# Kernel tuning notes

Measured on AMD Instinct MI355X. Metric: run time of the kernel, lower is better.

## Reference

```python
import jax, jax.numpy as jnp
import numpy as np

N = 50000      # nodes
E = 800000     # edges (before self-loops)
H = 4          # attention heads
C = 64         # hidden_dim per head
F_IN = 8       # node_features
NEG_SLOPE = 0.2  # PyG GATConv default


def setup_inputs() -> dict:
    key = jax.random.key(0)
    ks = jax.random.split(key, 16)
    def g(k, shape, fan_in):
        return (jax.random.normal(k, shape, jnp.float32) / np.sqrt(fan_in)).astype(jnp.float32)
    x = jax.random.normal(ks[0], (N, F_IN), jnp.float32)
    edge_index = jax.random.randint(ks[1], (2, E), 0, N, dtype=jnp.int32)
    # GATConv params: layer 0 maps F_IN->H*C, layers 1,2 map H*C->H*C
    W0 = g(ks[2], (F_IN, H * C), F_IN)
    Ws = g(ks[3], (2, H * C, H * C), H * C)
    att_src = g(ks[4], (3, H, C), C)
    att_dst = g(ks[5], (3, H, C), C)
    bconv = jnp.zeros((3, H * C), jnp.float32)
    # order / time predictor MLPs: Linear(256,64) -> ReLU -> Linear(64,1)
    ow1 = g(ks[6], (H * C, C), H * C); ob1 = jnp.zeros((C,), jnp.float32)
    ow2 = g(ks[7], (C, 1), C);         ob2 = jnp.zeros((1,), jnp.float32)
    tw1 = g(ks[8], (H * C, C), H * C); tb1 = jnp.zeros((C,), jnp.float32)
    tw2 = g(ks[9], (C, 1), C);         tb2 = jnp.zeros((1,), jnp.float32)
    return {"x": x, "edge_index": edge_index, "W0": W0, "Ws": Ws,
            "att_src": att_src, "att_dst": att_dst, "bconv": bconv,
            "ow1": ow1, "ob1": ob1, "ow2": ow2, "ob2": ob2,
            "tw1": tw1, "tb1": tb1, "tw2": tw2, "tb2": tb2}


def _gat_layer(h_in, src, dst, W, a_src, a_dst, b):
    """PyG-style GATConv (concat heads, eval mode, self-loops already in src/dst)."""
    h = (h_in @ W).reshape(N, H, C)                       # [N,H,C]
    al_s = jnp.einsum('nhc,hc->nh', h, a_src)             # [N,H]
    al_d = jnp.einsum('nhc,hc->nh', h, a_dst)             # [N,H]
    e = jax.nn.leaky_relu(al_s[src] + al_d[dst], NEG_SLOPE)  # [Etot,H]
    m = jax.ops.segment_max(e, dst, num_segments=N)       # segment-softmax over in-edges
    ee = jnp.exp(e - m[dst])
    den = jax.ops.segment_sum(ee, dst, num_segments=N)
    alpha = ee / den[dst]                                 # [Etot,H]
    out = jax.ops.segment_sum(h[src] * alpha[:, :, None], dst, num_segments=N)
    return out.reshape(N, H * C) + b


def reference(x, edge_index, W0, Ws, att_src, att_dst, bconv,
              ow1, ob1, ow2, ob2, tw1, tb1, tw2, tb2):
    loops = jnp.arange(N, dtype=edge_index.dtype)
    src = jnp.concatenate([edge_index[0], loops])
    dst = jnp.concatenate([edge_index[1], loops])
    h = _gat_layer(x, src, dst, W0, att_src[0], att_dst[0], bconv[0])
    h = jax.nn.relu(h)   # dropout is identity in eval
    h = _gat_layer(h, src, dst, Ws[0], att_src[1], att_dst[1], bconv[1])
    h = jax.nn.relu(h)
    h = _gat_layer(h, src, dst, Ws[1], att_src[2], att_dst[2], bconv[2])
    order_scores = jax.nn.relu(h @ ow1 + ob1) @ ow2 + ob2  # [N,1]
    time_scores = jax.nn.relu(h @ tw1 + tb1) @ tw2 + tb2   # [N,1]
    return (order_scores, time_scores)
```

## Files before the change

kernel.cpp:

```cpp
#include <hip/hip_runtime.h>
#include <hip/hip_bf16.h>
#include <hip/hip_fp16.h>

#define NN 50000
#define EE 800000
#define ET 850000
#define HH 4
#define CC 64
#define HC 256
#define DMAX 128

using f16v8 = __attribute__((ext_vector_type(8))) _Float16;
using f32v4 = __attribute__((ext_vector_type(4))) float;

__device__ __forceinline__ float4 cvt_h4(uint2 raw) {
    __half2 a = *reinterpret_cast<__half2*>(&raw.x);
    __half2 b = *reinterpret_cast<__half2*>(&raw.y);
    float2 fa = __half22float2(a), fb = __half22float2(b);
    return make_float4(fa.x, fa.y, fb.x, fb.y);
}

__global__ void k_bucket(const int* __restrict__ ei, int* __restrict__ cnt,
                         int* __restrict__ esrc) {
    int e = blockIdx.x * blockDim.x + threadIdx.x;
    if (e < ET) {
        int d, s;
        if (e < EE) { d = ei[EE + e]; s = ei[e]; }
        else        { d = e - EE;     s = e - EE; }
        int pos = atomicAdd(&cnt[d], 1);
        if (pos < DMAX) esrc[d * DMAX + pos] = s;
    }
}

__global__ void k_prep(const float* __restrict__ Ws,
                       const float* __restrict__ ow1, const float* __restrict__ tw1,
                       __half* __restrict__ Wt, __half* __restrict__ Wh) {
    int i = blockIdx.x * 256 + threadIdx.x;
    if (i < 2 * HC * HC) {
        int m = i >> 16;
        int n = (i >> 8) & 255;
        int k = i & 255;
        Wt[i] = __float2half(Ws[m * HC * HC + k * HC + n]);
    }
    int j = i - 2 * HC * HC;
    if (j >= 0 && j < 128 * HC) {
        int c = j >> 8;
        int k = j & 255;
        float v = (c < 64) ? ow1[k * CC + c] : tw1[k * CC + (c - 64)];
        Wh[j] = __float2half(v);
    }
}

#define G0_NODES 16
__global__ __launch_bounds__(256) void k_gemm0(const float* __restrict__ x,
                                               const float* __restrict__ W0,
                                               const float* __restrict__ asrc,
                                               const float* __restrict__ adst,
                                               __half* __restrict__ hg,
                                               float* __restrict__ al_s,
                                               float* __restrict__ al_d) {
    __shared__ float sx[G0_NODES * 8];
    int t = threadIdx.x;
    int n0 = blockIdx.x * G0_NODES;
    float w[8];
#pragma unroll
    for (int k = 0; k < 8; k++) w[k] = W0[k * HC + t];
    float as = asrc[t], ad = adst[t];
    int lane = t & 63, wv = t >> 6;
    if (t < G0_NODES * 8) sx[t] = x[(size_t)n0 * 8 + t];
    __syncthreads();
    for (int ni = 0; ni < G0_NODES; ni++) {
        int n = n0 + ni;
        float acc = 0.f;
#pragma unroll
        for (int k = 0; k < 8; k++) acc += sx[ni * 8 + k] * w[k];
        hg[(size_t)n * HC + t] = __float2half(acc);
        float s = acc * as, d = acc * ad;
        for (int off = 32; off > 0; off >>= 1) {
            s += __shfl_down(s, off, 64);
            d += __shfl_down(d, off, 64);
        }
        if (lane == 0) { al_s[n * HH + wv] = s; al_d[n * HH + wv] = d; }
    }
}

#define GM 128
#define GN 128
#define GK 64
__global__ __launch_bounds__(256) void k_gemmh(const __half* __restrict__ A,
                                               const __half* __restrict__ Bt,
                                               const float* __restrict__ asrc,
                                               const float* __restrict__ adst,
                                               __half* __restrict__ hg,
                                               float* __restrict__ al_s,
                                               float* __restrict__ al_d) {
    __shared__ __half As[GM][GK + 8];
    __shared__ __half Bs[GN][GK + 8];
    int t = threadIdx.x;
    int l = t & 63, wv = t >> 6;
    int wm = wv >> 1, wn = wv & 1;
    int row0 = blockIdx.x * GM;
    int col0 = blockIdx.y * GN;
    f32v4 acc[4][4] = {};
    const __half* Ab = A + (size_t)row0 * HC;
    const __half* Bb = Bt + (size_t)col0 * HC;
    int sr = t >> 3, sc = (t & 7) * 8;
    for (int k0 = 0; k0 < HC; k0 += GK) {
#pragma unroll
        for (int i = 0; i < 4; i++) {
            int rr = sr + i * 32;
            uint4 v = {0u, 0u, 0u, 0u};
            if (row0 + rr < NN) v = *(const uint4*)(Ab + (size_t)rr * HC + k0 + sc);
            *(uint4*)&As[rr][sc] = v;
            *(uint4*)&Bs[rr][sc] = *(const uint4*)(Bb + (size_t)rr * HC + k0 + sc);
        }
        __syncthreads();
#pragma unroll
        for (int kk = 0; kk < GK; kk += 32) {
            f16v8 af[4], bf[4];
#pragma unroll
            for (int i = 0; i < 4; i++)
                af[i] = *(const f16v8*)&As[wm * 64 + i * 16 + (l & 15)][kk + (l >> 4) * 8];
#pragma unroll
            for (int j = 0; j < 4; j++)
                bf[j] = *(const f16v8*)&Bs[wn * 64 + j * 16 + (l & 15)][kk + (l >> 4) * 8];
#pragma unroll
            for (int i = 0; i < 4; i++)
#pragma unroll
                for (int j = 0; j < 4; j++)
                    acc[i][j] = __builtin_amdgcn_mfma_f32_16x16x32_f16(af[i], bf[j], acc[i][j], 0, 0, 0);
        }
        __syncthreads();
    }
    int head = (col0 >> 6) + wn;
    float va[4], vd[4];
#pragma unroll
    for (int j = 0; j < 4; j++) {
        int c = j * 16 + (l & 15);
        va[j] = asrc[head * CC + c];
        vd[j] = adst[head * CC + c];
    }
    int cbase = col0 + wn * 64 + (l & 15);
#pragma unroll
    for (int i = 0; i < 4; i++) {
#pragma unroll
        for (int v = 0; v < 4; v++) {
            int r = row0 + wm * 64 + i * 16 + (l >> 4) * 4 + v;
            bool ok = (r < NN);
            float s = 0.f, d = 0.f;
#pragma unroll
            for (int j = 0; j < 4; j++) {
                float xv = acc[i][j][v];
                s += xv * va[j];
                d += xv * vd[j];
                if (ok) hg[(size_t)r * HC + cbase + j * 16] = __float2half(xv);
            }
            s += __shfl_xor(s, 8, 16); d += __shfl_xor(d, 8, 16);
            s += __shfl_xor(s, 4, 16); d += __shfl_xor(d, 4, 16);
            s += __shfl_xor(s, 2, 16); d += __shfl_xor(d, 2, 16);
            s += __shfl_xor(s, 1, 16); d += __shfl_xor(d, 1, 16);
            if (ok && (l & 15) == 0) {
                al_s[r * HH + head] = s;
                al_d[r * HH + head] = d;
            }
        }
    }
}

__global__ __launch_bounds__(256) void k_fagg(const int* __restrict__ cnt,
                                              const int* __restrict__ esrc,
                                              const float* __restrict__ al_s,
                                              const float* __restrict__ al_d,
                                              const __half* __restrict__ hg,
                                              const float* __restrict__ bias,
                                              __half* __restrict__ out, int do_relu) {
    __shared__ float s_p[4][HH][72];
    __shared__ int   s_src[4][64];
    int t = threadIdx.x;
    int wv = t >> 6, l = t & 63;
    int n = blockIdx.x * 4 + wv;
    int myh = l >> 4;
    int beg = n * DMAX;
    int end = beg + cnt[n];
    float4 ad = *(const float4*)&al_d[(size_t)n * HH];
    float den = 0.f;
    float4 acc = {0.f, 0.f, 0.f, 0.f};
    const __half* hgl = hg + l * 4;

    for (int off = beg; off < end; off += 64) {
        int csize = min(64, end - off);
        float4 pp = {0.f, 0.f, 0.f, 0.f};
        int s = 0;
        if (l < csize) {
            s = esrc[off + l];
            float4 as = *(const float4*)&al_s[(size_t)s * HH];
            float v;
            v = as.x + ad.x; pp.x = __expf((v > 0.f) ? v : 0.2f * v);
            v = as.y + ad.y; pp.y = __expf((v > 0.f) ? v : 0.2f * v);
            v = as.z + ad.z; pp.z = __expf((v > 0.f) ? v : 0.2f * v);
            v = as.w + ad.w; pp.w = __expf((v > 0.f) ? v : 0.2f * v);
        }
        s_src[wv][l] = s;
        s_p[wv][0][l] = pp.x;
        s_p[wv][1][l] = pp.y;
        s_p[wv][2][l] = pp.z;
        s_p[wv][3][l] = pp.w;
        const float* prow = s_p[wv][myh];
        const int*   srow = s_src[wv];
        int k = 0;
        for (; k + 8 <= csize; k += 8) {
            int si[8];
#pragma unroll
            for (int u = 0; u < 8; u++) si[u] = srow[k + u];
            uint2 rw[8];
#pragma unroll
            for (int u = 0; u < 8; u++) rw[u] = *(const uint2*)&hgl[(size_t)si[u] * HC];
            float p[8];
#pragma unroll
            for (int u = 0; u < 8; u++) p[u] = prow[k + u];
#pragma unroll
            for (int u = 0; u < 8; u++) {
                float4 v = cvt_h4(rw[u]);
                den += p[u];
                acc.x += p[u] * v.x;
                acc.y += p[u] * v.y;
                acc.z += p[u] * v.z;
                acc.w += p[u] * v.w;
            }
        }
        for (; k + 4 <= csize; k += 4) {
            int si[4];
#pragma unroll
            for (int u = 0; u < 4; u++) si[u] = srow[k + u];
            uint2 rw[4];
#pragma unroll
            for (int u = 0; u < 4; u++) rw[u] = *(const uint2*)&hgl[(size_t)si[u] * HC];
            float p[4];
#pragma unroll
            for (int u = 0; u < 4; u++) p[u] = prow[k + u];
#pragma unroll
            for (int u = 0; u < 4; u++) {
                float4 v = cvt_h4(rw[u]);
                den += p[u];
                acc.x += p[u] * v.x;
                acc.y += p[u] * v.y;
                acc.z += p[u] * v.z;
                acc.w += p[u] * v.w;
            }
        }
        for (; k < csize; k++) {
            float p = prow[k];
            float4 v = cvt_h4(*(const uint2*)&hgl[(size_t)srow[k] * HC]);
            den += p;
            acc.x += p * v.x; acc.y += p * v.y; acc.z += p * v.z; acc.w += p * v.w;
        }
    }

    float4 b = *(const float4*)&bias[l * 4];
    float inv = 1.f / den;
    float4 o;
    o.x = acc.x * inv + b.x; o.y = acc.y * inv + b.y;
    o.z = acc.z * inv + b.z; o.w = acc.w * inv + b.w;
    if (do_relu) {
        o.x = fmaxf(o.x, 0.f); o.y = fmaxf(o.y, 0.f);
        o.z = fmaxf(o.z, 0.f); o.w = fmaxf(o.w, 0.f);
    }
    union { __half h[4]; uint2 u; } pk;
    pk.h[0] = __float2half(o.x); pk.h[1] = __float2half(o.y);
    pk.h[2] = __float2half(o.z); pk.h[3] = __float2half(o.w);
    *(uint2*)&out[(size_t)n * HC + l * 4] = pk.u;
}

__global__ __launch_bounds__(256) void k_headh(const __half* __restrict__ A,
                                               const __half* __restrict__ Wh,
                                               const float* __restrict__ ob1,
                                               const float* __restrict__ ow2,
                                               const float* __restrict__ ob2,
                                               const float* __restrict__ tb1,
                                               const float* __restrict__ tw2,
                                               const float* __restrict__ tb2,
                                               float* __restrict__ out) {
    __shared__ __half As[GM][GK + 8];
    __shared__ __half Bs[GN][GK + 8];
    int t = threadIdx.x;
    int l = t & 63, wv = t >> 6;
    int wm = wv >> 1, wn = wv & 1;
    int row0 = blockIdx.x * GM;
    f32v4 acc[4][4] = {};
    const __half* Ab = A + (size_t)row0 * HC;
    int sr = t >> 3, sc = (t & 7) * 8;
    for (int k0 = 0; k0 < HC; k0 += GK) {
#pragma unroll
        for (int i = 0; i < 4; i++) {
            int rr = sr + i * 32;
            uint4 v = {0u, 0u, 0u, 0u};
            if (row0 + rr < NN) v = *(const uint4*)(Ab + (size_t)rr * HC + k0 + sc);
            *(uint4*)&As[rr][sc] = v;
            *(uint4*)&Bs[rr][sc] = *(const uint4*)(Wh + (size_t)rr * HC + k0 + sc);
        }
        __syncthreads();
#pragma unroll
        for (int kk = 0; kk < GK; kk += 32) {
            f16v8 af[4], bf[4];
#pragma unroll
            for (int i = 0; i < 4; i++)
                af[i] = *(const f16v8*)&As[wm * 64 + i * 16 + (l & 15)][kk + (l >> 4) * 8];
#pragma unroll
            for (int j = 0; j < 4; j++)
                bf[j] = *(const f16v8*)&Bs[wn * 64 + j * 16 + (l & 15)][kk + (l >> 4) * 8];
#pragma unroll
            for (int i = 0; i < 4; i++)
#pragma unroll
                for (int j = 0; j < 4; j++)
                    acc[i][j] = __builtin_amdgcn_mfma_f32_16x16x32_f16(af[i], bf[j], acc[i][j], 0, 0, 0);
        }
        __syncthreads();
    }
    float b1[4], w2[4];
#pragma unroll
    for (int j = 0; j < 4; j++) {
        int c = j * 16 + (l & 15);
        b1[j] = wn ? tb1[c] : ob1[c];
        w2[j] = wn ? tw2[c] : ow2[c];
    }
    float b2 = wn ? tb2[0] : ob2[0];
#pragma unroll
    for (int i = 0; i < 4; i++) {
#pragma unroll
        for (int v = 0; v < 4; v++) {
            int r = row0 + wm * 64 + i * 16 + (l >> 4) * 4 + v;
            float s = 0.f;
#pragma unroll
            for (int j = 0; j < 4; j++)
                s += fmaxf(acc[i][j][v] + b1[j], 0.f) * w2[j];
            s += __shfl_xor(s, 8, 16);
            s += __shfl_xor(s, 4, 16);
            s += __shfl_xor(s, 2, 16);
            s += __shfl_xor(s, 1, 16);
            if ((l & 15) == 0 && r < NN)
                out[(size_t)(wn ? NN : 0) + r] = s + b2;
        }
    }
}

extern "C" void kernel_launch(void* const* d_in, const int* in_sizes, int n_in,
                              void* d_out, int out_size, void* d_ws, size_t ws_size,
                              hipStream_t stream) {
    const float* x      = (const float*)d_in[0];
    const int*   ei     = (const int*)d_in[1];
    const float* W0     = (const float*)d_in[2];
    const float* Ws     = (const float*)d_in[3];
    const float* attsrc = (const float*)d_in[4];
    const float* attdst = (const float*)d_in[5];
    const float* bconv  = (const float*)d_in[6];
    const float* ow1 = (const float*)d_in[7];
    const float* ob1 = (const float*)d_in[8];
    const float* ow2 = (const float*)d_in[9];
    const float* ob2 = (const float*)d_in[10];
    const float* tw1 = (const float*)d_in[11];
    const float* tb1 = (const float*)d_in[12];
    const float* tw2 = (const float*)d_in[13];
    const float* tb2 = (const float*)d_in[14];
    float* outp = (float*)d_out;

    char* ws = (char*)d_ws;
    size_t off = 0;
    auto alloc = [&](size_t bytes) -> void* {
        void* p = ws + off;
        off += (bytes + 255) & ~(size_t)255;
        return p;
    };
    __half*   hA      = (__half*)alloc(sizeof(__half) * NN * HC);
    __half*   hB16    = (__half*)alloc(sizeof(__half) * NN * HC);
    float*    al_s    = (float*)alloc(sizeof(float) * NN * HH);
    float*    al_d    = (float*)alloc(sizeof(float) * NN * HH);
    int*      cnt     = (int*)alloc(sizeof(int) * NN);
    int*      esrc    = (int*)alloc(sizeof(int) * (size_t)NN * DMAX);
    __half*   Wt      = (__half*)alloc(sizeof(__half) * 2 * HC * HC);
    __half*   Wh      = (__half*)alloc(sizeof(__half) * 128 * HC);
    (void)ws_size; (void)in_sizes; (void)n_in; (void)out_size;

    hipMemsetAsync(cnt, 0, sizeof(int) * NN, stream);
    k_bucket<<<(ET + 255) / 256, 256, 0, stream>>>(ei, cnt, esrc);
    k_prep<<<(2 * HC * HC + 128 * HC + 255) / 256, 256, 0, stream>>>(Ws, ow1, tw1, Wt, Wh);

    for (int l = 0; l < 3; l++) {
        if (l == 0) {
            k_gemm0<<<NN / G0_NODES, 256, 0, stream>>>(x, W0, attsrc, attdst,
                                                       hA, al_s, al_d);
        } else {
            dim3 grid((NN + GM - 1) / GM, 2);
            k_gemmh<<<grid, 256, 0, stream>>>(hB16, Wt + (size_t)(l - 1) * HC * HC,
                                              attsrc + l * HC, attdst + l * HC,
                                              hA, al_s, al_d);
        }
        k_fagg<<<NN / 4, 256, 0, stream>>>(cnt, esrc, al_s, al_d, hA,
                                           bconv + l * HC, hB16, (l < 2) ? 1 : 0);
    }

    k_headh<<<(NN + GM - 1) / GM, 256, 0, stream>>>(hB16, Wh, ob1, ow2, ob2,
                                                    tb1, tw2, tb2, outp);
}
```

Before: 364.9 us.

## Build compact CSR with 16-bit sources and split aggregation by column slice

Replaces the fixed 128-slot padded bucket with a CSR built from a count histogram, an atomic-cursor offset assignment and a scatter pass. Source indices are stored as 16-bit values, and the histogram and offset steps are fused into the weight-prep and layer-0 GEMM kernels. The aggregation kernel now gives each block one 32-column slice for 16 nodes, with 8 edges handled in parallel per wavefront and combined by a shuffle reduction. This is meant to shrink edge-list memory, drop the degree cap, and spread gather work more evenly. In exchange it adds an extra edge pass and reduction overhead, and the order of sources within a node's edge list is no longer deterministic.

```diff
diff --git a/kernel.cpp b/kernel.cpp
--- a/kernel.cpp
+++ b/kernel.cpp
@@ -8,7 +8,6 @@
 #define HH 4
 #define CC 64
 #define HC 256
-#define DMAX 128
 
 using f16v8 = __attribute__((ext_vector_type(8))) _Float16;
 using f32v4 = __attribute__((ext_vector_type(4))) float;
@@ -20,22 +19,20 @@
     return make_float4(fa.x, fa.y, fb.x, fb.y);
 }
 
-__global__ void k_bucket(const int* __restrict__ ei, int* __restrict__ cnt,
-                         int* __restrict__ esrc) {
-    int e = blockIdx.x * blockDim.x + threadIdx.x;
-    if (e < ET) {
-        int d, s;
-        if (e < EE) { d = ei[EE + e]; s = ei[e]; }
-        else        { d = e - EE;     s = e - EE; }
-        int pos = atomicAdd(&cnt[d], 1);
-        if (pos < DMAX) esrc[d * DMAX + pos] = s;
-    }
-}
-
-__global__ void k_prep(const float* __restrict__ Ws,
-                       const float* __restrict__ ow1, const float* __restrict__ tw1,
-                       __half* __restrict__ Wt, __half* __restrict__ Wh) {
-    int i = blockIdx.x * 256 + threadIdx.x;
+#define HISTB 3321
+__global__ void k_hist_prep(const int* __restrict__ ei, int* __restrict__ cnt,
+                            const float* __restrict__ Ws,
+                            const float* __restrict__ ow1, const float* __restrict__ tw1,
+                            __half* __restrict__ Wt, __half* __restrict__ Wh) {
+    if (blockIdx.x < HISTB) {
+        int e = blockIdx.x * 256 + threadIdx.x;
+        if (e < ET) {
+            int d = (e < EE) ? ei[EE + e] : (e - EE);
+            atomicAdd(&cnt[d], 1);
+        }
+        return;
+    }
+    int i = (blockIdx.x - HISTB) * 256 + threadIdx.x;
     if (i < 2 * HC * HC) {
         int m = i >> 16;
         int n = (i >> 8) & 255;
@@ -51,17 +48,27 @@
     }
 }
 
+#define ASSIGNB 196
 #define G0_NODES 16
-__global__ __launch_bounds__(256) void k_gemm0(const float* __restrict__ x,
-                                               const float* __restrict__ W0,
-                                               const float* __restrict__ asrc,
-                                               const float* __restrict__ adst,
-                                               __half* __restrict__ hg,
-                                               float* __restrict__ al_s,
-                                               float* __restrict__ al_d) {
+__global__ __launch_bounds__(256) void k_assign_gemm0(
+        const int* __restrict__ cnt, int* __restrict__ row_ptr,
+        int* __restrict__ cur, int* __restrict__ cursor,
+        const float* __restrict__ x, const float* __restrict__ W0,
+        const float* __restrict__ asrc, const float* __restrict__ adst,
+        __half* __restrict__ hg, float* __restrict__ al_s,
+        float* __restrict__ al_d) {
+    if (blockIdx.x < ASSIGNB) {
+        int d = blockIdx.x * 256 + threadIdx.x;
+        if (d < NN) {
+            int off = atomicAdd(cursor, cnt[d]);
+            row_ptr[d] = off;
+            cur[d] = off;
+        }
+        return;
+    }
     __shared__ float sx[G0_NODES * 8];
     int t = threadIdx.x;
-    int n0 = blockIdx.x * G0_NODES;
+    int n0 = (blockIdx.x - ASSIGNB) * G0_NODES;
     float w[8];
 #pragma unroll
     for (int k = 0; k < 8; k++) w[k] = W0[k * HC + t];
@@ -81,6 +88,18 @@
             d += __shfl_down(d, off, 64);
         }
         if (lane == 0) { al_s[n * HH + wv] = s; al_d[n * HH + wv] = d; }
+    }
+}
+
+__global__ void k_scatter(const int* __restrict__ ei, int* __restrict__ cur,
+                          unsigned short* __restrict__ esrc) {
+    int e = blockIdx.x * blockDim.x + threadIdx.x;
+    if (e < ET) {
+        int d, s;
+        if (e < EE) { d = ei[EE + e]; s = ei[e]; }
+        else        { d = e - EE;     s = d; }
+        int pos = atomicAdd(&cur[d], 1);
+        esrc[pos] = (unsigned short)s;
     }
 }
 
@@ -168,107 +187,97 @@
 }
 
 __global__ __launch_bounds__(256) void k_fagg(const int* __restrict__ cnt,
-                                              const int* __restrict__ esrc,
+                                              const int* __restrict__ row_ptr,
+                                              const unsigned short* __restrict__ esrc,
                                               const float* __restrict__ al_s,
                                               const float* __restrict__ al_d,
                                               const __half* __restrict__ hg,
                                               const float* __restrict__ bias,
                                               __half* __restrict__ out, int do_relu) {
-    __shared__ float s_p[4][HH][72];
-    __shared__ int   s_src[4][64];
+    __shared__ float s_p[4][72];
+    __shared__ int   s_src[4][72];
     int t = threadIdx.x;
     int wv = t >> 6, l = t & 63;
-    int n = blockIdx.x * 4 + wv;
-    int myh = l >> 4;
-    int beg = n * DMAX;
-    int end = beg + cnt[n];
-    float4 ad = *(const float4*)&al_d[(size_t)n * HH];
-    float den = 0.f;
-    float4 acc = {0.f, 0.f, 0.f, 0.f};
-    const __half* hgl = hg + l * 4;
-
-    for (int off = beg; off < end; off += 64) {
-        int csize = min(64, end - off);
-        float4 pp = {0.f, 0.f, 0.f, 0.f};
-        int s = 0;
-        if (l < csize) {
-            s = esrc[off + l];
-            float4 as = *(const float4*)&al_s[(size_t)s * HH];
-            float v;
-            v = as.x + ad.x; pp.x = __expf((v > 0.f) ? v : 0.2f * v);
-            v = as.y + ad.y; pp.y = __expf((v > 0.f) ? v : 0.2f * v);
-            v = as.z + ad.z; pp.z = __expf((v > 0.f) ? v : 0.2f * v);
-            v = as.w + ad.w; pp.w = __expf((v > 0.f) ? v : 0.2f * v);
-        }
-        s_src[wv][l] = s;
-        s_p[wv][0][l] = pp.x;
-        s_p[wv][1][l] = pp.y;
-        s_p[wv][2][l] = pp.z;
-        s_p[wv][3][l] = pp.w;
-        const float* prow = s_p[wv][myh];
-        const int*   srow = s_src[wv];
-        int k = 0;
-        for (; k + 8 <= csize; k += 8) {
-            int si[8];
-#pragma unroll
-            for (int u = 0; u < 8; u++) si[u] = srow[k + u];
-            uint2 rw[8];
-#pragma unroll
-            for (int u = 0; u < 8; u++) rw[u] = *(const uint2*)&hgl[(size_t)si[u] * HC];
-            float p[8];
-#pragma unroll
-            for (int u = 0; u < 8; u++) p[u] = prow[k + u];
-#pragma unroll
-            for (int u = 0; u < 8; u++) {
-                float4 v = cvt_h4(rw[u]);
-                den += p[u];
-                acc.x += p[u] * v.x;
-                acc.y += p[u] * v.y;
-                acc.z += p[u] * v.z;
-                acc.w += p[u] * v.w;
-            }
-        }
-        for (; k + 4 <= csize; k += 4) {
-            int si[4];
-#pragma unroll
-            for (int u = 0; u < 4; u++) si[u] = srow[k + u];
-            uint2 rw[4];
-#pragma unroll
-            for (int u = 0; u < 4; u++) rw[u] = *(const uint2*)&hgl[(size_t)si[u] * HC];
-            float p[4];
-#pragma unroll
-            for (int u = 0; u < 4; u++) p[u] = prow[k + u];
-#pragma unroll
-            for (int u = 0; u < 4; u++) {
-                float4 v = cvt_h4(rw[u]);
-                den += p[u];
-                acc.x += p[u] * v.x;
-                acc.y += p[u] * v.y;
-                acc.z += p[u] * v.z;
-                acc.w += p[u] * v.w;
-            }
-        }
-        for (; k < csize; k++) {
-            float p = prow[k];
-            float4 v = cvt_h4(*(const uint2*)&hgl[(size_t)srow[k] * HC]);
-            den += p;
-            acc.x += p * v.x; acc.y += p * v.y; acc.z += p * v.z; acc.w += p * v.w;
-        }
-    }
-
-    float4 b = *(const float4*)&bias[l * 4];
-    float inv = 1.f / den;
-    float4 o;
-    o.x = acc.x * inv + b.x; o.y = acc.y * inv + b.y;
-    o.z = acc.z * inv + b.z; o.w = acc.w * inv + b.w;
-    if (do_relu) {
-        o.x = fmaxf(o.x, 0.f); o.y = fmaxf(o.y, 0.f);
-        o.z = fmaxf(o.z, 0.f); o.w = fmaxf(o.w, 0.f);
-    }
-    union { __half h[4]; uint2 u; } pk;
-    pk.h[0] = __float2half(o.x); pk.h[1] = __float2half(o.y);
-    pk.h[2] = __float2half(o.z); pk.h[3] = __float2half(o.w);
-    *(uint2*)&out[(size_t)n * HC + l * 4] = pk.u;
+    int sh = blockIdx.x & 7;
+    int grp = blockIdx.x >> 3;
+    int h = sh >> 1;
+    int colbase = sh * 32;
+    int eg = l >> 3, cq = l & 7;
+    const __half* hgl = hg + colbase + cq * 4;
+    float4 b4 = *(const float4*)&bias[colbase + cq * 4];
+
+    for (int ni = 0; ni < 4; ni++) {
+        int n = grp * 16 + wv * 4 + ni;
+        int beg = row_ptr[n], deg = cnt[n];
+        float ad = al_d[n * HH + h];
+        float den = 0.f;
+        float4 acc = {0.f, 0.f, 0.f, 0.f};
+        for (int off = 0; off < deg; off += 64) {
+            int csize = min(64, deg - off);
+            float p = 0.f; int s = 0;
+            if (l < csize) {
+                s = (int)esrc[beg + off + l];
+                float v = al_s[s * HH + h] + ad;
+                p = __expf((v > 0.f) ? v : 0.2f * v);
+            }
+            s_src[wv][l] = s;
+            s_p[wv][l] = p;
+            const float* prow = s_p[wv];
+            const int*   srow = s_src[wv];
+            int k = 0;
+            for (; k + 32 <= csize; k += 32) {
+                int si[4]; float pv[4]; uint2 rw[4];
+#pragma unroll
+                for (int u = 0; u < 4; u++) {
+                    int e = k + u * 8 + eg;
+                    si[u] = srow[e]; pv[u] = prow[e];
+                }
+#pragma unroll
+                for (int u = 0; u < 4; u++)
+                    rw[u] = *(const uint2*)&hgl[(size_t)si[u] * HC];
+#pragma unroll
+                for (int u = 0; u < 4; u++) {
+                    float4 v = cvt_h4(rw[u]);
+                    den += pv[u];
+                    acc.x += pv[u] * v.x; acc.y += pv[u] * v.y;
+                    acc.z += pv[u] * v.z; acc.w += pv[u] * v.w;
+                }
+            }
+            for (; k < csize; k += 8) {
+                int e = k + eg;
+                bool ok = (e < csize);
+                float pv = ok ? prow[e] : 0.f;
+                int si = ok ? srow[e] : 0;
+                uint2 rw = *(const uint2*)&hgl[(size_t)si * HC];
+                float4 v = cvt_h4(rw);
+                den += pv;
+                acc.x += pv * v.x; acc.y += pv * v.y;
+                acc.z += pv * v.z; acc.w += pv * v.w;
+            }
+        }
+#pragma unroll
+        for (int dlt = 8; dlt < 64; dlt <<= 1) {
+            den   += __shfl_xor(den, dlt, 64);
+            acc.x += __shfl_xor(acc.x, dlt, 64);
+            acc.y += __shfl_xor(acc.y, dlt, 64);
+            acc.z += __shfl_xor(acc.z, dlt, 64);
+            acc.w += __shfl_xor(acc.w, dlt, 64);
+        }
+        if (eg == 0) {
+            float inv = 1.f / den;
+            float4 o;
+            o.x = acc.x * inv + b4.x; o.y = acc.y * inv + b4.y;
+            o.z = acc.z * inv + b4.z; o.w = acc.w * inv + b4.w;
+            if (do_relu) {
+                o.x = fmaxf(o.x, 0.f); o.y = fmaxf(o.y, 0.f);
+                o.z = fmaxf(o.z, 0.f); o.w = fmaxf(o.w, 0.f);
+            }
+            union { __half h4[4]; uint2 u; } pk;
+            pk.h4[0] = __float2half(o.x); pk.h4[1] = __float2half(o.y);
+            pk.h4[2] = __float2half(o.z); pk.h4[3] = __float2half(o.w);
+            *(uint2*)&out[(size_t)n * HC + colbase + cq * 4] = pk.u;
+        }
+    }
 }
 
 __global__ __launch_bounds__(256) void k_headh(const __half* __restrict__ A,
@@ -370,32 +379,36 @@
         off += (bytes + 255) & ~(size_t)255;
         return p;
     };
-    __half*   hA      = (__half*)alloc(sizeof(__half) * NN * HC);
-    __half*   hB16    = (__half*)alloc(sizeof(__half) * NN * HC);
-    float*    al_s    = (float*)alloc(sizeof(float) * NN * HH);
-    float*    al_d    = (float*)alloc(sizeof(float) * NN * HH);
-    int*      cnt     = (int*)alloc(sizeof(int) * NN);
-    int*      esrc    = (int*)alloc(sizeof(int) * (size_t)NN * DMAX);
-    __half*   Wt      = (__half*)alloc(sizeof(__half) * 2 * HC * HC);
-    __half*   Wh      = (__half*)alloc(sizeof(__half) * 128 * HC);
+    __half*         hA      = (__half*)alloc(sizeof(__half) * NN * HC);
+    __half*         hB16    = (__half*)alloc(sizeof(__half) * NN * HC);
+    float*          al_s    = (float*)alloc(sizeof(float) * NN * HH);
+    float*          al_d    = (float*)alloc(sizeof(float) * NN * HH);
+    int*            cnt     = (int*)alloc(sizeof(int) * NN);
+    int*            row_ptr = (int*)alloc(sizeof(int) * NN);
+    int*            cur     = (int*)alloc(sizeof(int) * NN);
+    int*            cursor  = (int*)alloc(sizeof(int));
+    unsigned short* esrc    = (unsigned short*)alloc(sizeof(unsigned short) * ET);
+    __half*         Wt      = (__half*)alloc(sizeof(__half) * 2 * HC * HC);
+    __half*         Wh      = (__half*)alloc(sizeof(__half) * 128 * HC);
     (void)ws_size; (void)in_sizes; (void)n_in; (void)out_size;
 
     hipMemsetAsync(cnt, 0, sizeof(int) * NN, stream);
-    k_bucket<<<(ET + 255) / 256, 256, 0, stream>>>(ei, cnt, esrc);
-    k_prep<<<(2 * HC * HC + 128 * HC + 255) / 256, 256, 0, stream>>>(Ws, ow1, tw1, Wt, Wh);
+    hipMemsetAsync(cursor, 0, sizeof(int), stream);
+    k_hist_prep<<<HISTB + 640, 256, 0, stream>>>(ei, cnt, Ws, ow1, tw1, Wt, Wh);
+    k_assign_gemm0<<<ASSIGNB + NN / G0_NODES, 256, 0, stream>>>(
+        cnt, row_ptr, cur, cursor, x, W0, attsrc, attdst, hA, al_s, al_d);
+    k_scatter<<<(ET + 255) / 256, 256, 0, stream>>>(ei, cur, esrc);
 
     for (int l = 0; l < 3; l++) {
-        if (l == 0) {
-            k_gemm0<<<NN / G0_NODES, 256, 0, stream>>>(x, W0, attsrc, attdst,
-                                                       hA, al_s, al_d);
-        } else {
+        if (l > 0) {
             dim3 grid((NN + GM - 1) / GM, 2);
             k_gemmh<<<grid, 256, 0, stream>>>(hB16, Wt + (size_t)(l - 1) * HC * HC,
                                               attsrc + l * HC, attdst + l * HC,
                                               hA, al_s, al_d);
         }
-        k_fagg<<<NN / 4, 256, 0, stream>>>(cnt, esrc, al_s, al_d, hA,
-                                           bconv + l * HC, hB16, (l < 2) ? 1 : 0);
+        k_fagg<<<(NN / 16) * 8, 256, 0, stream>>>(cnt, row_ptr, esrc, al_s, al_d,
+                                                  hA, bconv + l * HC, hB16,
+                                                  (l < 2) ? 1 : 0);
     }
 
     k_headh<<<(NN + GM - 1) / GM, 256, 0, stream>>>(hB16, Wh, ob1, ow2, ob2,
```

New measurement: 646.7 us. 77.2% more time.

## Build compact CSR adjacency with 16-bit sources instead of fixed-degree buckets

Applied to the files above, without the earlier changes.

Replaces the fixed DMAX=128 per-node bucket array with a compact CSR built from a histogram, an atomic-cursor offset assignment and a scatter pass. Source indices are stored as unsigned short to halve index bandwidth. The histogram is fused with weight prep, and offset assignment is fused with the layer-0 GEMM, to cut launches. This adds one extra pass over the edges and gives non-monotonic row order, which hurts locality. The 16-bit indices only hold while node ids stay below 65536.

```diff
diff --git a/kernel.cpp b/kernel.cpp
--- a/kernel.cpp
+++ b/kernel.cpp
@@ -8,7 +8,6 @@
 #define HH 4
 #define CC 64
 #define HC 256
-#define DMAX 128
 
 using f16v8 = __attribute__((ext_vector_type(8))) _Float16;
 using f32v4 = __attribute__((ext_vector_type(4))) float;
@@ -20,22 +19,20 @@
     return make_float4(fa.x, fa.y, fb.x, fb.y);
 }
 
-__global__ void k_bucket(const int* __restrict__ ei, int* __restrict__ cnt,
-                         int* __restrict__ esrc) {
-    int e = blockIdx.x * blockDim.x + threadIdx.x;
-    if (e < ET) {
-        int d, s;
-        if (e < EE) { d = ei[EE + e]; s = ei[e]; }
-        else        { d = e - EE;     s = e - EE; }
-        int pos = atomicAdd(&cnt[d], 1);
-        if (pos < DMAX) esrc[d * DMAX + pos] = s;
-    }
-}
-
-__global__ void k_prep(const float* __restrict__ Ws,
-                       const float* __restrict__ ow1, const float* __restrict__ tw1,
-                       __half* __restrict__ Wt, __half* __restrict__ Wh) {
-    int i = blockIdx.x * 256 + threadIdx.x;
+#define HISTB 3321
+__global__ void k_hist_prep(const int* __restrict__ ei, int* __restrict__ cnt,
+                            const float* __restrict__ Ws,
+                            const float* __restrict__ ow1, const float* __restrict__ tw1,
+                            __half* __restrict__ Wt, __half* __restrict__ Wh) {
+    if (blockIdx.x < HISTB) {
+        int e = blockIdx.x * 256 + threadIdx.x;
+        if (e < ET) {
+            int d = (e < EE) ? ei[EE + e] : (e - EE);
+            atomicAdd(&cnt[d], 1);
+        }
+        return;
+    }
+    int i = (blockIdx.x - HISTB) * 256 + threadIdx.x;
     if (i < 2 * HC * HC) {
         int m = i >> 16;
         int n = (i >> 8) & 255;
@@ -51,17 +48,27 @@
     }
 }
 
+#define ASSIGNB 196
 #define G0_NODES 16
-__global__ __launch_bounds__(256) void k_gemm0(const float* __restrict__ x,
-                                               const float* __restrict__ W0,
-                                               const float* __restrict__ asrc,
-                                               const float* __restrict__ adst,
-                                               __half* __restrict__ hg,
-                                               float* __restrict__ al_s,
-                                               float* __restrict__ al_d) {
+__global__ __launch_bounds__(256) void k_assign_gemm0(
+        const int* __restrict__ cnt, int* __restrict__ row_ptr,
+        int* __restrict__ cur, int* __restrict__ cursor,
+        const float* __restrict__ x, const float* __restrict__ W0,
+        const float* __restrict__ asrc, const float* __restrict__ adst,
+        __half* __restrict__ hg, float* __restrict__ al_s,
+        float* __restrict__ al_d) {
+    if (blockIdx.x < ASSIGNB) {
+        int d = blockIdx.x * 256 + threadIdx.x;
+        if (d < NN) {
+            int off = atomicAdd(cursor, cnt[d]);
+            row_ptr[d] = off;
+            cur[d] = off;
+        }
+        return;
+    }
     __shared__ float sx[G0_NODES * 8];
     int t = threadIdx.x;
-    int n0 = blockIdx.x * G0_NODES;
+    int n0 = (blockIdx.x - ASSIGNB) * G0_NODES;
     float w[8];
 #pragma unroll
     for (int k = 0; k < 8; k++) w[k] = W0[k * HC + t];
@@ -81,6 +88,18 @@
             d += __shfl_down(d, off, 64);
         }
         if (lane == 0) { al_s[n * HH + wv] = s; al_d[n * HH + wv] = d; }
+    }
+}
+
+__global__ void k_scatter(const int* __restrict__ ei, int* __restrict__ cur,
+                          unsigned short* __restrict__ esrc) {
+    int e = blockIdx.x * blockDim.x + threadIdx.x;
+    if (e < ET) {
+        int d, s;
+        if (e < EE) { d = ei[EE + e]; s = ei[e]; }
+        else        { d = e - EE;     s = d; }
+        int pos = atomicAdd(&cur[d], 1);
+        esrc[pos] = (unsigned short)s;
     }
 }
 
@@ -168,7 +187,8 @@
 }
 
 __global__ __launch_bounds__(256) void k_fagg(const int* __restrict__ cnt,
-                                              const int* __restrict__ esrc,
+                                              const int* __restrict__ row_ptr,
+                                              const unsigned short* __restrict__ esrc,
                                               const float* __restrict__ al_s,
                                               const float* __restrict__ al_d,
                                               const __half* __restrict__ hg,
@@ -180,7 +200,7 @@
     int wv = t >> 6, l = t & 63;
     int n = blockIdx.x * 4 + wv;
     int myh = l >> 4;
-    int beg = n * DMAX;
+    int beg = row_ptr[n];
     int end = beg + cnt[n];
     float4 ad = *(const float4*)&al_d[(size_t)n * HH];
     float den = 0.f;
@@ -192,7 +212,7 @@
         float4 pp = {0.f, 0.f, 0.f, 0.f};
         int s = 0;
         if (l < csize) {
-            s = esrc[off + l];
+            s = (int)esrc[(size_t)off + l];
             float4 as = *(const float4*)&al_s[(size_t)s * HH];
             float v;
             v = as.x + ad.x; pp.x = __expf((v > 0.f) ? v : 0.2f * v);
@@ -370,32 +390,36 @@
         off += (bytes + 255) & ~(size_t)255;
         return p;
     };
-    __half*   hA      = (__half*)alloc(sizeof(__half) * NN * HC);
-    __half*   hB16    = (__half*)alloc(sizeof(__half) * NN * HC);
-    float*    al_s    = (float*)alloc(sizeof(float) * NN * HH);
-    float*    al_d    = (float*)alloc(sizeof(float) * NN * HH);
-    int*      cnt     = (int*)alloc(sizeof(int) * NN);
-    int*      esrc    = (int*)alloc(sizeof(int) * (size_t)NN * DMAX);
-    __half*   Wt      = (__half*)alloc(sizeof(__half) * 2 * HC * HC);
-    __half*   Wh      = (__half*)alloc(sizeof(__half) * 128 * HC);
+    __half*         hA      = (__half*)alloc(sizeof(__half) * NN * HC);
+    __half*         hB16    = (__half*)alloc(sizeof(__half) * NN * HC);
+    float*          al_s    = (float*)alloc(sizeof(float) * NN * HH);
+    float*          al_d    = (float*)alloc(sizeof(float) * NN * HH);
+    int*            cnt     = (int*)alloc(sizeof(int) * NN);
+    int*            row_ptr = (int*)alloc(sizeof(int) * NN);
+    int*            cur     = (int*)alloc(sizeof(int) * NN);
+    int*            cursor  = (int*)alloc(sizeof(int));
+    unsigned short* esrc    = (unsigned short*)alloc(sizeof(unsigned short) * ET);
+    __half*         Wt      = (__half*)alloc(sizeof(__half) * 2 * HC * HC);
+    __half*         Wh      = (__half*)alloc(sizeof(__half) * 128 * HC);
     (void)ws_size; (void)in_sizes; (void)n_in; (void)out_size;
 
     hipMemsetAsync(cnt, 0, sizeof(int) * NN, stream);
-    k_bucket<<<(ET + 255) / 256, 256, 0, stream>>>(ei, cnt, esrc);
-    k_prep<<<(2 * HC * HC + 128 * HC + 255) / 256, 256, 0, stream>>>(Ws, ow1, tw1, Wt, Wh);
+    hipMemsetAsync(cursor, 0, sizeof(int), stream);
+    k_hist_prep<<<HISTB + 640, 256, 0, stream>>>(ei, cnt, Ws, ow1, tw1, Wt, Wh);
+    k_assign_gemm0<<<ASSIGNB + NN / G0_NODES, 256, 0, stream>>>(
+        cnt, row_ptr, cur, cursor, x, W0, attsrc, attdst, hA, al_s, al_d);
+    k_scatter<<<(ET + 255) / 256, 256, 0, stream>>>(ei, cur, esrc);
 
     for (int l = 0; l < 3; l++) {
-        if (l == 0) {
-            k_gemm0<<<NN / G0_NODES, 256, 0, stream>>>(x, W0, attsrc, attdst,
-                                                       hA, al_s, al_d);
-        } else {
+        if (l > 0) {
             dim3 grid((NN + GM - 1) / GM, 2);
             k_gemmh<<<grid, 256, 0, stream>>>(hB16, Wt + (size_t)(l - 1) * HC * HC,
                                               attsrc + l * HC, attdst + l * HC,
                                               hA, al_s, al_d);
         }
-        k_fagg<<<NN / 4, 256, 0, stream>>>(cnt, esrc, al_s, al_d, hA,
-                                           bconv + l * HC, hB16, (l < 2) ? 1 : 0);
+        k_fagg<<<NN / 4, 256, 0, stream>>>(cnt, row_ptr, esrc, al_s, al_d,
+                                           hA, bconv + l * HC, hB16,
+                                           (l < 2) ? 1 : 0);
     }
 
     k_headh<<<(NN + GM - 1) / GM, 256, 0, stream>>>(hB16, Wh, ob1, ow2, ob2,
```

New measurement: 386.3 us. 5.9% more time.
